# Optimization experiments

Measured on AMD Instinct MI355X. Metric: run time of the kernel, lower is better.

The kernel has to match this reference:

```python
import jax, jax.numpy as jnp
import numpy as np

B, S, I, H, P = 4096, 1024, 6, 128, 50  # batch, seq_len, input_size, hidden_size, predict_size


def setup_inputs() -> dict:
    key = jax.random.key(0)
    ks = jax.random.split(key, 12)
    k = 1.0 / np.sqrt(H)  # torch LSTM default init: U(-1/sqrt(H), 1/sqrt(H))
    u = lambda kk, shape: jax.random.uniform(kk, shape, jnp.float32, -k, k)
    # xavier_uniform for fc: bound = sqrt(6/(fan_in+fan_out))
    xb = np.sqrt(6.0 / (H + I))
    return {
        "x": jax.random.normal(ks[0], (B, S, I), jnp.float32),
        "w_ih0": u(ks[1], (4 * H, I)),
        "w_hh0": u(ks[2], (4 * H, H)),
        "b_ih0": u(ks[3], (4 * H,)),
        "b_hh0": u(ks[4], (4 * H,)),
        "w_ih1": u(ks[5], (4 * H, H)),
        "w_hh1": u(ks[6], (4 * H, H)),
        "b_ih1": u(ks[7], (4 * H,)),
        "b_hh1": u(ks[8], (4 * H,)),
        "fc_w": jax.random.uniform(ks[9], (I, H), jnp.float32, -xb, xb),
        "fc_b": jnp.full((I,), 0.01, jnp.float32),
    }


def _cell(xt, h, c, w_ih, w_hh, b):
    # gates: [i, f, g, o] stacked along last dim (torch order)
    g = xt @ w_ih.T + h @ w_hh.T + b
    i, f, gg, o = jnp.split(g, 4, axis=-1)
    c = jax.nn.sigmoid(f) * c + jax.nn.sigmoid(i) * jnp.tanh(gg)
    h = jax.nn.sigmoid(o) * jnp.tanh(c)
    return h, c


def reference(x, w_ih0, w_hh0, b_ih0, b_hh0, w_ih1, w_hh1, b_ih1, b_hh1, fc_w, fc_b):
    b0 = b_ih0 + b_hh0
    b1 = b_ih1 + b_hh1
    z = jnp.zeros((x.shape[0], H), x.dtype)

    def two_layer_step(carry, xt):
        h0, c0, h1, c1 = carry
        h0, c0 = _cell(xt, h0, c0, w_ih0, w_hh0, b0)
        h1, c1 = _cell(h0, h1, c1, w_ih1, w_hh1, b1)
        return (h0, c0, h1, c1), None

    # encode the input sequence; last top-layer output == final h1
    (h0, c0, h1, c1), _ = jax.lax.scan(two_layer_step, (z, z, z, z),
                                       jnp.swapaxes(x, 0, 1))  # (S,B,I)
    cur = jnp.tanh(h1 @ fc_w.T + fc_b)  # (B, I)

    def ar_step(carry, _):
        h0, c0, h1, c1, cur = carry
        h0, c0 = _cell(cur, h0, c0, w_ih0, w_hh0, b0)
        h1, c1 = _cell(h0, h1, c1, w_ih1, w_hh1, b1)
        pred = jnp.tanh(h1 @ fc_w.T + fc_b)
        return (h0, c0, h1, c1, pred), pred

    _, preds = jax.lax.scan(ar_step, (h0, c0, h1, c1, cur), None, length=P)
    return jnp.swapaxes(preds, 0, 1)  # (B, P, I)
```

## Files before the change

### kernel.cpp

```cpp
#include <hip/hip_runtime.h>

#define SEQ 1024
#define ISZ 6
#define HSZ 128
#define PRED 50
#define MROW 16
#define HP   136
#define XCH  8
#define WSB  131072

using f32x4  = __attribute__((ext_vector_type(4))) float;
using bf16x8 = __attribute__((ext_vector_type(8))) short;

__device__ __forceinline__ short f2bf(float f){
  union { float f; unsigned u; } v; v.f = f;
  unsigned r = v.u + 0x7FFFu + ((v.u >> 16) & 1u);
  return (short)(r >> 16);
}
__device__ __forceinline__ float bf2f(unsigned short us){
  union { unsigned u; float f; } v; v.u = ((unsigned)us) << 16; return v.f;
}
__device__ __forceinline__ float sigf(float x){
  float e = __builtin_amdgcn_exp2f(x * -1.4426950408889634f);
  return __builtin_amdgcn_rcpf(1.0f + e);
}
__device__ __forceinline__ float tanhf_(float x){
  float e = __builtin_amdgcn_exp2f(x * 2.8853900817779268f);
  return 1.0f - 2.0f * __builtin_amdgcn_rcpf(1.0f + e);
}

#define PIN(v) asm volatile("" : "+v"(v))

template<int PRECVT>
__global__
__attribute__((amdgpu_flat_work_group_size(512, 512)))
void lstm_ar(
    const float* __restrict__ x,
    const float* __restrict__ w_ih0, const float* __restrict__ w_hh0,
    const float* __restrict__ b_ih0, const float* __restrict__ b_hh0,
    const float* __restrict__ w_ih1, const float* __restrict__ w_hh1,
    const float* __restrict__ b_ih1, const float* __restrict__ b_hh1,
    const float* __restrict__ fc_w, const float* __restrict__ fc_b,
    float* __restrict__ out, unsigned short* __restrict__ wsb)
{
  __shared__ short s_whh1[65536];
  __shared__ short s_h0[2][MROW*HP];
  __shared__ short s_h1[MROW*HP];
  __shared__ short s_x[(XCH+1)*MROW*8];
  __shared__ short s_wih0[512*8];
  __shared__ float s_bias[2*512];
  __shared__ float s_fcb[8];
  __shared__ short s_zpad[8];

  const int tid  = threadIdx.x;
  const int wv   = tid >> 6;
  const int lane = tid & 63;
  const int l15  = lane & 15;
  const int lq   = lane >> 4;
  const int u    = wv*16 + l15;
  const int row0 = blockIdx.x * MROW;
  char* const whh1b = (char*)s_whh1;

  for (int i = tid; i < 2*MROW*HP; i += 512) (&s_h0[0][0])[i] = 0;
  for (int i = tid; i < MROW*HP;   i += 512) s_h1[i] = 0;
  for (int i = tid; i < (XCH+1)*MROW*8; i += 512) s_x[i] = 0;
  if (tid < 8){ s_zpad[tid] = 0; s_fcb[tid] = (tid < 6) ? fc_b[tid] : 0.f; }
  {
    #pragma unroll
    for (int k = 0; k < 6; k++) s_wih0[tid*8 + k] = f2bf(w_ih0[tid*6 + k]);
    s_wih0[tid*8 + 6] = 0; s_wih0[tid*8 + 7] = 0;
  }
  for (int i = tid; i < 1024; i += 512)
    s_bias[i] = (i < 512) ? (b_ih0[i] + b_hh0[i]) : (b_ih1[i-512] + b_hh1[i-512]);

  for (int i = tid; i < 32768; i += 512){
    const int c = i >> 6, kp = i & 63;
    const unsigned lo = (unsigned short)f2bf(w_hh1[c*128 + 2*kp]);
    const unsigned hi = (unsigned short)f2bf(w_hh1[c*128 + 2*kp + 1]);
    *(unsigned*)(whh1b + ((i*4) ^ ((c & 7) << 4))) = lo | (hi << 16);
  }

  if (PRECVT){
    #pragma unroll
    for (int g = 0; g < 4; g++){
      const int c = g*128 + u;
      #pragma unroll
      for (int kt = 0; kt < 4; kt++){
        const float* wp = w_hh0 + c*HSZ + kt*32 + lq*8;
        bf16x8 f;
        #pragma unroll
        for (int i = 0; i < 8; i++) f[i] = f2bf(wp[i]);
        *(bf16x8*)(wsb + (((wv*4 + g)*4 + kt)*64 + lane)*8) = f;
      }
    }
  }

  bf16x8 wih1f[4][4];
  #pragma unroll
  for (int g = 0; g < 4; g++){
    const int c = g*128 + u;
    #pragma unroll
    for (int kt = 0; kt < 4; kt++){
      const float* wp = w_ih1 + c*HSZ + kt*32 + lq*8;
      bf16x8 f;
      #pragma unroll
      for (int i = 0; i < 8; i++) f[i] = f2bf(wp[i]);
      wih1f[g][kt] = f;
    }
  }

  float c0[4] = {0.f,0.f,0.f,0.f}, c1[4] = {0.f,0.f,0.f,0.f};
  volatile const float* vb = s_bias;
  __syncthreads();

  for (int t = 0; t < SEQ + PRED; ++t){
    #pragma unroll
    for (int g = 0; g < 4; g++){
      #pragma unroll
      for (int kt = 0; kt < 4; kt++) PIN(wih1f[g][kt]);
    }

    if (t < SEQ && (t & (XCH-1)) == 0){
      for (int i = tid; i < XCH*MROW*ISZ; i += 512){
        const int r = i / (XCH*ISZ), rem = i % (XCH*ISZ);
        const int ts = rem / ISZ, k = rem % ISZ;
        s_x[(ts*MROW + r)*8 + k] =
          f2bf(x[(size_t)(row0 + r)*(SEQ*ISZ) + (size_t)(t + ts)*ISZ + k]);
      }
      __syncthreads();
    }
    const int tt = (t < SEQ) ? (t & (XCH-1)) : XCH;
    const int pb = t & 1, qb = pb ^ 1;

    const bf16x8 ax = *(const bf16x8*)((lq == 0) ? (s_x + (tt*MROW + l15)*8) : s_zpad);
    f32x4 acc[4];
    #pragma unroll
    for (int g = 0; g < 4; g++){
      const bf16x8 bw = *(const bf16x8*)((lq == 0) ? (s_wih0 + (g*128 + u)*8) : s_zpad);
      const float bg = vb[g*128 + u];
      f32x4 ci; ci[0] = bg; ci[1] = bg; ci[2] = bg; ci[3] = bg;
      acc[g] = __builtin_amdgcn_mfma_f32_16x16x32_bf16(ax, bw, ci, 0, 0, 0);
    }
    #pragma unroll
    for (int kt = 0; kt < 4; kt++){
      bf16x8 stg[4];
      if (PRECVT){
        #pragma unroll
        for (int g = 0; g < 4; g++)
          stg[g] = *(const bf16x8*)(wsb + (((wv*4 + g)*4 + kt)*64 + lane)*8);
      } else {
        #pragma unroll
        for (int g = 0; g < 4; g++){
          const float* wp = w_hh0 + (g*128 + u)*HSZ + kt*32 + lq*8;
          bf16x8 f;
          #pragma unroll
          for (int i = 0; i < 8; i++) f[i] = f2bf(wp[i]);
          stg[g] = f;
        }
      }
      const bf16x8 a = *(const bf16x8*)(s_h0[qb] + l15*HP + (kt*4 + lq)*8);
      #pragma unroll
      for (int g = 0; g < 4; g++)
        acc[g] = __builtin_amdgcn_mfma_f32_16x16x32_bf16(a, stg[g], acc[g], 0, 0, 0);
    }
    #pragma unroll
    for (int j = 0; j < 4; j++){
      const float iv = sigf(acc[0][j]);
      const float fv = sigf(acc[1][j]);
      const float gv = tanhf_(acc[2][j]);
      const float ov = sigf(acc[3][j]);
      c0[j] = fv*c0[j] + iv*gv;
      const float h = ov * tanhf_(c0[j]);
      s_h0[pb][(lq*4 + j)*HP + u] = f2bf(h);
    }
    __syncthreads();

    #pragma unroll
    for (int g = 0; g < 4; g++){
      const float bg = vb[512 + g*128 + u];
      acc[g][0] = bg; acc[g][1] = bg; acc[g][2] = bg; acc[g][3] = bg;
    }
    #pragma unroll
    for (int kt = 0; kt < 4; kt++){
      const bf16x8 a = *(const bf16x8*)(s_h0[pb] + l15*HP + (kt*4 + lq)*8);
      #pragma unroll
      for (int g = 0; g < 4; g++)
        acc[g] = __builtin_amdgcn_mfma_f32_16x16x32_bf16(a, wih1f[g][kt], acc[g], 0, 0, 0);
    }
    #pragma unroll
    for (int kt = 0; kt < 4; kt++){
      const bf16x8 a = *(const bf16x8*)(s_h1 + l15*HP + (kt*4 + lq)*8);
      #pragma unroll
      for (int g = 0; g < 4; g++){
        const int c = g*128 + u;
        const bf16x8 b = *(const bf16x8*)(whh1b +
            ((c*256 + (kt*4 + lq)*16) ^ ((u & 7) << 4)));
        acc[g] = __builtin_amdgcn_mfma_f32_16x16x32_bf16(a, b, acc[g], 0, 0, 0);
      }
    }
    __syncthreads();
    const bool dofc = (t >= SEQ - 1);
    #pragma unroll
    for (int j = 0; j < 4; j++){
      const float iv = sigf(acc[0][j]);
      const float fv = sigf(acc[1][j]);
      const float gv = tanhf_(acc[2][j]);
      const float ov = sigf(acc[3][j]);
      c1[j] = fv*c1[j] + iv*gv;
      const float h = ov * tanhf_(c1[j]);
      s_h1[(lq*4 + j)*HP + u] = f2bf(h);
    }

    if (dofc){
      __syncthreads();
      if (tid < 96){
        const int r = tid / 6, ii = tid % 6;
        float sacc = 0.f;
        #pragma unroll 4
        for (int kk = 0; kk < 128; kk++)
          sacc += bf2f((unsigned short)s_h1[r*HP + kk]) * fc_w[ii*128 + kk];
        const float pred = tanhf_(s_fcb[ii] + sacc);
        s_x[(XCH*MROW + r)*8 + ii] = f2bf(pred);
        if (t >= SEQ)
          out[(size_t)(row0 + r)*(PRED*ISZ) + (size_t)(t - SEQ)*ISZ + ii] = pred;
      }
      __syncthreads();
    }
  }
}

extern "C" void kernel_launch(void* const* d_in, const int* in_sizes, int n_in,
                              void* d_out, int out_size, void* d_ws, size_t ws_size,
                              hipStream_t stream) {
  const float* x     = (const float*)d_in[0];
  const float* w_ih0 = (const float*)d_in[1];
  const float* w_hh0 = (const float*)d_in[2];
  const float* b_ih0 = (const float*)d_in[3];
  const float* b_hh0 = (const float*)d_in[4];
  const float* w_ih1 = (const float*)d_in[5];
  const float* w_hh1 = (const float*)d_in[6];
  const float* b_ih1 = (const float*)d_in[7];
  const float* b_hh1 = (const float*)d_in[8];
  const float* fc_w  = (const float*)d_in[9];
  const float* fc_b  = (const float*)d_in[10];
  float* out = (float*)d_out;
  unsigned short* wsb = (unsigned short*)d_ws;

  const int Btot = in_sizes[0] / (SEQ * ISZ);
  const int nblk = Btot / MROW;

  if (ws_size >= (size_t)WSB)
    lstm_ar<1><<<dim3(nblk), dim3(512), 0, stream>>>(
        x, w_ih0, w_hh0, b_ih0, b_hh0, w_ih1, w_hh1, b_ih1, b_hh1,
        fc_w, fc_b, out, wsb);
  else
    lstm_ar<0><<<dim3(nblk), dim3(512), 0, stream>>>(
        x, w_ih0, w_hh0, b_ih0, b_hh0, w_ih1, w_hh1, b_ih1, b_hh1,
        fc_w, fc_b, out, wsb);
}
```

Before: 3.207 ms.

## Split LSTM layers into producer/consumer blocks pipelined through global-memory rings

```diff
diff --git a/kernel.cpp b/kernel.cpp
--- a/kernel.cpp
+++ b/kernel.cpp
@@ -7,7 +7,31 @@
 #define MROW 16
 #define HP   136
 #define XCH  8
-#define WSB  131072
+#define NS   2
+#define TSTEPS (SEQ + PRED)
+
+#define F_H0   ((size_t)0)
+#define F_CUR  ((size_t)32768)
+#define F_CONS ((size_t)65536)
+#define F_ABT  ((size_t)98304)
+#define FLAGBYTES ((size_t)98432)
+#define R_H0   FLAGBYTES
+#define R_CUR  (R_H0 + (size_t)256*NS*4096)
+#define R_W1   (R_CUR + (size_t)256*NS*256)
+#define WS_NEED (R_W1 + (size_t)65536)
+
+#define OW1    0
+#define OLAND  65536
+#define OH1    69888
+#define OFCW   74240
+#define OCT    77312
+#define OFCB   77568
+#define OZP1   77600
+#define OH0    0
+#define OX     8704
+#define OWIH0  10752
+#define OZP0   18944
+#define POOLB  77632
 
 using f32x4  = __attribute__((ext_vector_type(4))) float;
 using bf16x8 = __attribute__((ext_vector_type(8))) short;
@@ -28,13 +52,304 @@
   float e = __builtin_amdgcn_exp2f(x * 2.8853900817779268f);
   return 1.0f - 2.0f * __builtin_amdgcn_rcpf(1.0f + e);
 }
-
 #define PIN(v) asm volatile("" : "+v"(v))
+
+__device__ __forceinline__ int aldf(const int* p){
+  return __hip_atomic_load(p, __ATOMIC_ACQUIRE, __HIP_MEMORY_SCOPE_AGENT);
+}
+__device__ __forceinline__ void astf(int* p, int v){
+  __hip_atomic_store(p, v, __ATOMIC_RELEASE, __HIP_MEMORY_SCOPE_AGENT);
+}
+__device__ __forceinline__ unsigned long long ald64(const void* p){
+  return __hip_atomic_load((const unsigned long long*)p, __ATOMIC_RELAXED, __HIP_MEMORY_SCOPE_AGENT);
+}
+__device__ __forceinline__ void ast64(void* p, unsigned long long v){
+  __hip_atomic_store((unsigned long long*)p, v, __ATOMIC_RELAXED, __HIP_MEMORY_SCOPE_AGENT);
+}
+__device__ __forceinline__ void ast32(void* p, unsigned v){
+  __hip_atomic_store((unsigned*)p, v, __ATOMIC_RELAXED, __HIP_MEMORY_SCOPE_AGENT);
+}
+__device__ __forceinline__ void waitge(const int* f, int v, int* abt){
+  if (threadIdx.x == 0){
+    int n = 0;
+    while (aldf(f) < v){
+      if (aldf(abt)) break;
+      __builtin_amdgcn_s_sleep(8);
+      if (++n > (1 << 21)){ astf(abt, 1); break; }
+    }
+  }
+  __syncthreads();
+}
+
+__global__
+__attribute__((amdgpu_flat_work_group_size(512, 512)))
+void lstm_pipe(
+    const float* __restrict__ x,
+    const float* __restrict__ w_ih0, const float* __restrict__ w_hh0,
+    const float* __restrict__ b_ih0, const float* __restrict__ b_hh0,
+    const float* __restrict__ w_ih1, const float* __restrict__ w_hh1,
+    const float* __restrict__ b_ih1, const float* __restrict__ b_hh1,
+    const float* __restrict__ fc_w, const float* __restrict__ fc_b,
+    float* __restrict__ out, char* __restrict__ ws)
+{
+  __shared__ __align__(16) char pool[POOLB];
+
+  const int tid  = threadIdx.x;
+  const int wv   = tid >> 6;
+  const int lane = tid & 63;
+  const int l15  = lane & 15;
+  const int lq   = lane >> 4;
+  const int u    = wv*16 + l15;
+  const int type = blockIdx.x >> 8;
+  const int p    = blockIdx.x & 255;
+  const int row0 = p * MROW;
+
+  int* h0f     = (int*)(ws + F_H0   + (size_t)p*128);
+  int* curf    = (int*)(ws + F_CUR  + (size_t)p*128);
+  int* consf   = (int*)(ws + F_CONS + (size_t)p*128);
+  int* abt     = (int*)(ws + F_ABT);
+  char* h0ring = ws + R_H0  + (size_t)p*(NS*4096);
+  char* curring= ws + R_CUR + (size_t)p*(NS*256);
+  short* w1p   = (short*)(ws + R_W1);
+
+  if (type == 0){
+    short* s_h0   = (short*)(pool + OH0);
+    short* s_x    = (short*)(pool + OX);
+    short* s_wih0 = (short*)(pool + OWIH0);
+    short* s_zp   = (short*)(pool + OZP0);
+
+    for (int i = tid; i < 2*MROW*HP; i += 512) s_h0[i] = 0;
+    for (int i = tid; i < XCH*MROW*8; i += 512) s_x[i] = 0;
+    if (tid < 8) s_zp[tid] = 0;
+    {
+      #pragma unroll
+      for (int k = 0; k < 6; k++) s_wih0[tid*8 + k] = f2bf(w_ih0[tid*6 + k]);
+      s_wih0[tid*8 + 6] = 0; s_wih0[tid*8 + 7] = 0;
+    }
+    bf16x8 whh0f[4][4];
+    float bias0[4];
+    #pragma unroll
+    for (int g = 0; g < 4; g++){
+      const int c = g*128 + u;
+      bias0[g] = b_ih0[c] + b_hh0[c];
+      #pragma unroll
+      for (int kt = 0; kt < 4; kt++){
+        const float* wp = w_hh0 + c*HSZ + kt*32 + lq*8;
+        bf16x8 f;
+        #pragma unroll
+        for (int i = 0; i < 8; i++) f[i] = f2bf(wp[i]);
+        whh0f[g][kt] = f;
+      }
+    }
+    float c0[4] = {0.f,0.f,0.f,0.f};
+    __syncthreads();
+
+    for (int t = 0; t < TSTEPS; ++t){
+      #pragma unroll
+      for (int g = 0; g < 4; g++){
+        #pragma unroll
+        for (int kt = 0; kt < 4; kt++) PIN(whh0f[g][kt]);
+      }
+      if (t >= NS) waitge(consf, t - NS + 1, abt);
+
+      bf16x8 ax;
+      if (t < SEQ){
+        if ((t & (XCH-1)) == 0){
+          for (int i = tid; i < XCH*MROW*ISZ; i += 512){
+            const int r = i / (XCH*ISZ), rem = i % (XCH*ISZ);
+            const int ts = rem / ISZ, k = rem % ISZ;
+            s_x[(ts*MROW + r)*8 + k] =
+              f2bf(x[(size_t)(row0 + r)*(SEQ*ISZ) + (size_t)(t + ts)*ISZ + k]);
+          }
+          __syncthreads();
+        }
+        ax = *(const bf16x8*)((lq == 0) ? (s_x + ((t & (XCH-1))*MROW + l15)*8) : s_zp);
+      } else {
+        waitge(curf, t - SEQ + 1, abt);
+        if (lq == 0){
+          const char* cp = curring + ((t - SEQ) % NS)*256 + l15*16;
+          union { unsigned long long q[2]; bf16x8 v; } uu;
+          uu.q[0] = ald64(cp); uu.q[1] = ald64(cp + 8);
+          ax = uu.v;
+        } else ax = *(const bf16x8*)s_zp;
+      }
+
+      const int pb = t & 1, qb = pb ^ 1;
+      short* h0q = s_h0 + qb*(MROW*HP);
+      short* h0p = s_h0 + pb*(MROW*HP);
+      f32x4 acc[4];
+      #pragma unroll
+      for (int g = 0; g < 4; g++){
+        const bf16x8 bw = *(const bf16x8*)((lq == 0) ? (s_wih0 + (g*128 + u)*8) : s_zp);
+        f32x4 ci; ci[0]=bias0[g]; ci[1]=bias0[g]; ci[2]=bias0[g]; ci[3]=bias0[g];
+        acc[g] = __builtin_amdgcn_mfma_f32_16x16x32_bf16(ax, bw, ci, 0, 0, 0);
+      }
+      #pragma unroll
+      for (int kt = 0; kt < 4; kt++){
+        const bf16x8 a = *(const bf16x8*)(h0q + l15*HP + (kt*4 + lq)*8);
+        #pragma unroll
+        for (int g = 0; g < 4; g++)
+          acc[g] = __builtin_amdgcn_mfma_f32_16x16x32_bf16(a, whh0f[g][kt], acc[g], 0, 0, 0);
+      }
+      #pragma unroll
+      for (int j = 0; j < 4; j++){
+        const float iv = sigf(acc[0][j]);
+        const float fv = sigf(acc[1][j]);
+        const float gv = tanhf_(acc[2][j]);
+        const float ov = sigf(acc[3][j]);
+        c0[j] = fv*c0[j] + iv*gv;
+        const float h = ov * tanhf_(c0[j]);
+        h0p[(lq*4 + j)*HP + u] = f2bf(h);
+      }
+      __syncthreads();
+      {
+        unsigned long long v = *(const unsigned long long*)(h0p + (tid >> 5)*HP + (tid & 31)*4);
+        ast64(h0ring + (t % NS)*4096 + tid*8, v);
+      }
+      __syncthreads();
+      if (tid == 0) astf(h0f, t + 1);
+    }
+  } else {
+    char*  w1l   = pool + OW1;
+    short* s_land= (short*)(pool + OLAND);
+    short* s_h1  = (short*)(pool + OH1);
+    float* s_fcw = (float*)(pool + OFCW);
+    short* s_ct  = (short*)(pool + OCT);
+    float* s_fcb = (float*)(pool + OFCB);
+
+    for (int i = tid; i < 16384; i += 512){
+      const int c = i >> 5, kp = i & 31;
+      const unsigned lo = (unsigned short)f2bf(w_ih1[c*128 + 2*kp]);
+      const unsigned hi = (unsigned short)f2bf(w_ih1[c*128 + 2*kp + 1]);
+      *(unsigned*)(w1l + ((i*4) ^ ((c & 7) << 4))) = lo | (hi << 16);
+    }
+    #pragma unroll
+    for (int g = 0; g < 4; g++){
+      const int c = g*128 + u;
+      #pragma unroll
+      for (int ktl = 0; ktl < 2; ktl++){
+        const float* wp = w_ih1 + c*HSZ + (2 + ktl)*32 + lq*8;
+        bf16x8 f;
+        #pragma unroll
+        for (int i = 0; i < 8; i++) f[i] = f2bf(wp[i]);
+        *(bf16x8*)(w1p + (((wv*4 + g)*2 + ktl)*64 + lane)*8) = f;
+      }
+    }
+    bf16x8 whh1f[4][4];
+    float bias1[4];
+    #pragma unroll
+    for (int g = 0; g < 4; g++){
+      const int c = g*128 + u;
+      bias1[g] = b_ih1[c] + b_hh1[c];
+      #pragma unroll
+      for (int kt = 0; kt < 4; kt++){
+        const float* wp = w_hh1 + c*HSZ + kt*32 + lq*8;
+        bf16x8 f;
+        #pragma unroll
+        for (int i = 0; i < 8; i++) f[i] = f2bf(wp[i]);
+        whh1f[g][kt] = f;
+      }
+    }
+    for (int i = tid; i < MROW*HP; i += 512) s_h1[i] = 0;
+    for (int i = tid; i < ISZ*HSZ; i += 512) s_fcw[i] = fc_w[i];
+    if (tid < 8) s_fcb[tid] = (tid < 6) ? fc_b[tid] : 0.f;
+    if (tid < MROW*8) s_ct[tid] = 0;
+    float c1[4] = {0.f,0.f,0.f,0.f};
+    __syncthreads();
+
+    for (int t = 0; t < TSTEPS; ++t){
+      #pragma unroll
+      for (int g = 0; g < 4; g++){
+        #pragma unroll
+        for (int kt = 0; kt < 4; kt++) PIN(whh1f[g][kt]);
+      }
+      waitge(h0f, t + 1, abt);
+      {
+        unsigned long long v = ald64(h0ring + (t % NS)*4096 + tid*8);
+        *(unsigned long long*)(s_land + (tid >> 5)*HP + (tid & 31)*4) = v;
+      }
+      __syncthreads();
+      if (tid == 0) astf(consf, t + 1);
+
+      bf16x8 sA[4], sB[4];
+      #pragma unroll
+      for (int g = 0; g < 4; g++){
+        sA[g] = *(const bf16x8*)(w1p + (((wv*4 + g)*2 + 0)*64 + lane)*8);
+        sB[g] = *(const bf16x8*)(w1p + (((wv*4 + g)*2 + 1)*64 + lane)*8);
+      }
+      f32x4 acc[4];
+      #pragma unroll
+      for (int g = 0; g < 4; g++){
+        acc[g][0]=bias1[g]; acc[g][1]=bias1[g]; acc[g][2]=bias1[g]; acc[g][3]=bias1[g];
+      }
+      #pragma unroll
+      for (int kt = 0; kt < 2; kt++){
+        const bf16x8 a = *(const bf16x8*)(s_land + l15*HP + (kt*4 + lq)*8);
+        #pragma unroll
+        for (int g = 0; g < 4; g++){
+          const int c = g*128 + u;
+          const bf16x8 b = *(const bf16x8*)(w1l +
+              ((c*128 + (kt*4 + lq)*16) ^ ((u & 7) << 4)));
+          acc[g] = __builtin_amdgcn_mfma_f32_16x16x32_bf16(a, b, acc[g], 0, 0, 0);
+        }
+      }
+      #pragma unroll
+      for (int kt = 0; kt < 4; kt++){
+        const bf16x8 a = *(const bf16x8*)(s_h1 + l15*HP + (kt*4 + lq)*8);
+        #pragma unroll
+        for (int g = 0; g < 4; g++)
+          acc[g] = __builtin_amdgcn_mfma_f32_16x16x32_bf16(a, whh1f[g][kt], acc[g], 0, 0, 0);
+      }
+      {
+        const bf16x8 a2 = *(const bf16x8*)(s_land + l15*HP + (2*4 + lq)*8);
+        #pragma unroll
+        for (int g = 0; g < 4; g++)
+          acc[g] = __builtin_amdgcn_mfma_f32_16x16x32_bf16(a2, sA[g], acc[g], 0, 0, 0);
+        const bf16x8 a3 = *(const bf16x8*)(s_land + l15*HP + (3*4 + lq)*8);
+        #pragma unroll
+        for (int g = 0; g < 4; g++)
+          acc[g] = __builtin_amdgcn_mfma_f32_16x16x32_bf16(a3, sB[g], acc[g], 0, 0, 0);
+      }
+      __syncthreads();
+      const bool dofc = (t >= SEQ - 1);
+      #pragma unroll
+      for (int j = 0; j < 4; j++){
+        const float iv = sigf(acc[0][j]);
+        const float fv = sigf(acc[1][j]);
+        const float gv = tanhf_(acc[2][j]);
+        const float ov = sigf(acc[3][j]);
+        c1[j] = fv*c1[j] + iv*gv;
+        const float h = ov * tanhf_(c1[j]);
+        s_h1[(lq*4 + j)*HP + u] = f2bf(h);
+      }
+      if (dofc){
+        __syncthreads();
+        if (tid < 96){
+          const int r = tid / 6, ii = tid % 6;
+          float sacc = 0.f;
+          #pragma unroll 4
+          for (int kk = 0; kk < 128; kk++)
+            sacc += bf2f((unsigned short)s_h1[r*HP + kk]) * s_fcw[ii*128 + kk];
+          const float pred = tanhf_(s_fcb[ii] + sacc);
+          s_ct[r*8 + ii] = f2bf(pred);
+          if (t >= SEQ)
+            out[(size_t)(row0 + r)*(PRED*ISZ) + (size_t)(t - SEQ)*ISZ + ii] = pred;
+        }
+        if (tid < 16){ s_ct[tid*8 + 6] = 0; s_ct[tid*8 + 7] = 0; }
+        __syncthreads();
+        if (tid < 64)
+          ast32(curring + ((t - (SEQ-1)) % NS)*256 + tid*4, ((unsigned*)s_ct)[tid]);
+        __syncthreads();
+        if (tid == 0) astf(curf, t - SEQ + 2);
+      }
+    }
+  }
+}
 
 template<int PRECVT>
 __global__
 __attribute__((amdgpu_flat_work_group_size(512, 512)))
-void lstm_ar(
+void lstm_fb(
     const float* __restrict__ x,
     const float* __restrict__ w_ih0, const float* __restrict__ w_hh0,
     const float* __restrict__ b_ih0, const float* __restrict__ b_hh0,
@@ -72,14 +387,12 @@
   }
   for (int i = tid; i < 1024; i += 512)
     s_bias[i] = (i < 512) ? (b_ih0[i] + b_hh0[i]) : (b_ih1[i-512] + b_hh1[i-512]);
-
   for (int i = tid; i < 32768; i += 512){
     const int c = i >> 6, kp = i & 63;
     const unsigned lo = (unsigned short)f2bf(w_hh1[c*128 + 2*kp]);
     const unsigned hi = (unsigned short)f2bf(w_hh1[c*128 + 2*kp + 1]);
     *(unsigned*)(whh1b + ((i*4) ^ ((c & 7) << 4))) = lo | (hi << 16);
   }
-
   if (PRECVT){
     #pragma unroll
     for (int g = 0; g < 4; g++){
@@ -94,7 +407,6 @@
       }
     }
   }
-
   bf16x8 wih1f[4][4];
   #pragma unroll
   for (int g = 0; g < 4; g++){
@@ -108,18 +420,16 @@
       wih1f[g][kt] = f;
     }
   }
-
   float c0[4] = {0.f,0.f,0.f,0.f}, c1[4] = {0.f,0.f,0.f,0.f};
   volatile const float* vb = s_bias;
   __syncthreads();
 
-  for (int t = 0; t < SEQ + PRED; ++t){
+  for (int t = 0; t < TSTEPS; ++t){
     #pragma unroll
     for (int g = 0; g < 4; g++){
       #pragma unroll
       for (int kt = 0; kt < 4; kt++) PIN(wih1f[g][kt]);
     }
-
     if (t < SEQ && (t & (XCH-1)) == 0){
       for (int i = tid; i < XCH*MROW*ISZ; i += 512){
         const int r = i / (XCH*ISZ), rem = i % (XCH*ISZ);
@@ -210,7 +520,6 @@
       const float h = ov * tanhf_(c1[j]);
       s_h1[(lq*4 + j)*HP + u] = f2bf(h);
     }
-
     if (dofc){
       __syncthreads();
       if (tid < 96){
@@ -244,17 +553,23 @@
   const float* fc_w  = (const float*)d_in[9];
   const float* fc_b  = (const float*)d_in[10];
   float* out = (float*)d_out;
-  unsigned short* wsb = (unsigned short*)d_ws;
-
-  const int Btot = in_sizes[0] / (SEQ * ISZ);
-  const int nblk = Btot / MROW;
-
-  if (ws_size >= (size_t)WSB)
-    lstm_ar<1><<<dim3(nblk), dim3(512), 0, stream>>>(
+
+  int nb = 0;
+  hipError_t oe = hipOccupancyMaxActiveBlocksPerMultiprocessor(&nb, lstm_pipe, 512, 0);
+  const bool pipe_ok = (oe == hipSuccess) && (nb >= 2) && (ws_size >= WS_NEED);
+
+  if (pipe_ok){
+    hipMemsetAsync(d_ws, 0, FLAGBYTES, stream);
+    lstm_pipe<<<dim3(512), dim3(512), 0, stream>>>(
         x, w_ih0, w_hh0, b_ih0, b_hh0, w_ih1, w_hh1, b_ih1, b_hh1,
-        fc_w, fc_b, out, wsb);
-  else
-    lstm_ar<0><<<dim3(nblk), dim3(512), 0, stream>>>(
+        fc_w, fc_b, out, (char*)d_ws);
+  } else if (ws_size >= (size_t)131072){
+    lstm_fb<1><<<dim3(256), dim3(512), 0, stream>>>(
         x, w_ih0, w_hh0, b_ih0, b_hh0, w_ih1, w_hh1, b_ih1, b_hh1,
-        fc_w, fc_b, out, wsb);
-}
+        fc_w, fc_b, out, (unsigned short*)d_ws);
+  } else {
+    lstm_fb<0><<<dim3(256), dim3(512), 0, stream>>>(
+        x, w_ih0, w_hh0, b_ih0, b_hh0, w_ih1, w_hh1, b_ih1, b_hh1,
+        fc_w, fc_b, out, (unsigned short*)d_ws);
+  }
+}
```

After: 3.207 ms. About the same (-0.0%).

## Double-buffer layer-1 hidden state and overlap its recurrent matmul with layer 0

Applied to the files above, without the earlier changes.

```diff
diff --git a/kernel.cpp b/kernel.cpp
--- a/kernel.cpp
+++ b/kernel.cpp
@@ -7,7 +7,11 @@
 #define MROW 16
 #define HP   136
 #define XCH  8
-#define WSB  131072
+#define TSTEPS (SEQ + PRED)
+
+#define W0OFF 0
+#define W1OFF 65536
+#define WS_NEED ((size_t)196608)
 
 using f32x4  = __attribute__((ext_vector_type(4))) float;
 using bf16x8 = __attribute__((ext_vector_type(8))) short;
@@ -28,13 +32,12 @@
   float e = __builtin_amdgcn_exp2f(x * 2.8853900817779268f);
   return 1.0f - 2.0f * __builtin_amdgcn_rcpf(1.0f + e);
 }
-
 #define PIN(v) asm volatile("" : "+v"(v))
 
 template<int PRECVT>
 __global__
 __attribute__((amdgpu_flat_work_group_size(512, 512)))
-void lstm_ar(
+void lstm_m2(
     const float* __restrict__ x,
     const float* __restrict__ w_ih0, const float* __restrict__ w_hh0,
     const float* __restrict__ b_ih0, const float* __restrict__ b_hh0,
@@ -43,14 +46,14 @@
     const float* __restrict__ fc_w, const float* __restrict__ fc_b,
     float* __restrict__ out, unsigned short* __restrict__ wsb)
 {
-  __shared__ short s_whh1[65536];
-  __shared__ short s_h0[2][MROW*HP];
-  __shared__ short s_h1[MROW*HP];
-  __shared__ short s_x[(XCH+1)*MROW*8];
-  __shared__ short s_wih0[512*8];
-  __shared__ float s_bias[2*512];
+  __shared__ __align__(16) short s_whh1[65536];
+  __shared__ __align__(16) short s_h0[2][MROW*HP];
+  __shared__ __align__(16) short s_h1[2][MROW*HP];
+  __shared__ __align__(16) short s_x[(XCH+1)*MROW*8];
+  __shared__ __align__(16) short s_wih0[512*8];
+  __shared__ __align__(16) float s_bias[1024];
   __shared__ float s_fcb[8];
-  __shared__ short s_zpad[8];
+  __shared__ __align__(16) short s_zpad[8];
 
   const int tid  = threadIdx.x;
   const int wv   = tid >> 6;
@@ -60,9 +63,11 @@
   const int u    = wv*16 + l15;
   const int row0 = blockIdx.x * MROW;
   char* const whh1b = (char*)s_whh1;
+  unsigned short* const w0p = wsb + W0OFF;
+  unsigned short* const w1p = wsb + W1OFF;
 
   for (int i = tid; i < 2*MROW*HP; i += 512) (&s_h0[0][0])[i] = 0;
-  for (int i = tid; i < MROW*HP;   i += 512) s_h1[i] = 0;
+  for (int i = tid; i < 2*MROW*HP; i += 512) (&s_h1[0][0])[i] = 0;
   for (int i = tid; i < (XCH+1)*MROW*8; i += 512) s_x[i] = 0;
   if (tid < 8){ s_zpad[tid] = 0; s_fcb[tid] = (tid < 6) ? fc_b[tid] : 0.f; }
   {
@@ -72,14 +77,12 @@
   }
   for (int i = tid; i < 1024; i += 512)
     s_bias[i] = (i < 512) ? (b_ih0[i] + b_hh0[i]) : (b_ih1[i-512] + b_hh1[i-512]);
-
   for (int i = tid; i < 32768; i += 512){
     const int c = i >> 6, kp = i & 63;
     const unsigned lo = (unsigned short)f2bf(w_hh1[c*128 + 2*kp]);
     const unsigned hi = (unsigned short)f2bf(w_hh1[c*128 + 2*kp + 1]);
     *(unsigned*)(whh1b + ((i*4) ^ ((c & 7) << 4))) = lo | (hi << 16);
   }
-
   if (PRECVT){
     #pragma unroll
     for (int g = 0; g < 4; g++){
@@ -90,17 +93,24 @@
         bf16x8 f;
         #pragma unroll
         for (int i = 0; i < 8; i++) f[i] = f2bf(wp[i]);
-        *(bf16x8*)(wsb + (((wv*4 + g)*4 + kt)*64 + lane)*8) = f;
-      }
-    }
-  }
-
-  bf16x8 wih1f[4][4];
+        *(bf16x8*)(w0p + (((wv*4 + g)*4 + kt)*64 + lane)*8) = f;
+      }
+      #pragma unroll
+      for (int ktl = 0; ktl < 2; ktl++){
+        const float* wp = w_ih1 + c*HSZ + (2 + ktl)*32 + lq*8;
+        bf16x8 f;
+        #pragma unroll
+        for (int i = 0; i < 8; i++) f[i] = f2bf(wp[i]);
+        *(bf16x8*)(w1p + (((wv*4 + g)*2 + ktl)*64 + lane)*8) = f;
+      }
+    }
+  }
+  bf16x8 wih1f[4][2];
   #pragma unroll
   for (int g = 0; g < 4; g++){
     const int c = g*128 + u;
     #pragma unroll
-    for (int kt = 0; kt < 4; kt++){
+    for (int kt = 0; kt < 2; kt++){
       const float* wp = w_ih1 + c*HSZ + kt*32 + lq*8;
       bf16x8 f;
       #pragma unroll
@@ -113,12 +123,9 @@
   volatile const float* vb = s_bias;
   __syncthreads();
 
-  for (int t = 0; t < SEQ + PRED; ++t){
-    #pragma unroll
-    for (int g = 0; g < 4; g++){
-      #pragma unroll
-      for (int kt = 0; kt < 4; kt++) PIN(wih1f[g][kt]);
-    }
+  for (int t = 0; t < TSTEPS; ++t){
+    #pragma unroll
+    for (int g = 0; g < 4; g++){ PIN(wih1f[g][0]); PIN(wih1f[g][1]); }
 
     if (t < SEQ && (t & (XCH-1)) == 0){
       for (int i = tid; i < XCH*MROW*ISZ; i += 512){
@@ -131,15 +138,23 @@
     }
     const int tt = (t < SEQ) ? (t & (XCH-1)) : XCH;
     const int pb = t & 1, qb = pb ^ 1;
+    short* const h0q = &s_h0[qb][0];
+    short* const h0p = &s_h0[pb][0];
+    short* const h1q = &s_h1[qb][0];
+    short* const h1p = &s_h1[pb][0];
+
+    float b0t[4], b1t[4];
+    #pragma unroll
+    for (int g = 0; g < 4; g++){ b0t[g] = vb[g*128 + u]; b1t[g] = vb[512 + g*128 + u]; }
 
     const bf16x8 ax = *(const bf16x8*)((lq == 0) ? (s_x + (tt*MROW + l15)*8) : s_zpad);
-    f32x4 acc[4];
+    f32x4 acc0[4], acc1[4];
     #pragma unroll
     for (int g = 0; g < 4; g++){
       const bf16x8 bw = *(const bf16x8*)((lq == 0) ? (s_wih0 + (g*128 + u)*8) : s_zpad);
-      const float bg = vb[g*128 + u];
-      f32x4 ci; ci[0] = bg; ci[1] = bg; ci[2] = bg; ci[3] = bg;
-      acc[g] = __builtin_amdgcn_mfma_f32_16x16x32_bf16(ax, bw, ci, 0, 0, 0);
+      f32x4 ci; ci[0]=b0t[g]; ci[1]=b0t[g]; ci[2]=b0t[g]; ci[3]=b0t[g];
+      acc0[g] = __builtin_amdgcn_mfma_f32_16x16x32_bf16(ax, bw, ci, 0, 0, 0);
+      acc1[g][0]=b1t[g]; acc1[g][1]=b1t[g]; acc1[g][2]=b1t[g]; acc1[g][3]=b1t[g];
     }
     #pragma unroll
     for (int kt = 0; kt < 4; kt++){
@@ -147,7 +162,7 @@
       if (PRECVT){
         #pragma unroll
         for (int g = 0; g < 4; g++)
-          stg[g] = *(const bf16x8*)(wsb + (((wv*4 + g)*4 + kt)*64 + lane)*8);
+          stg[g] = *(const bf16x8*)(w0p + (((wv*4 + g)*4 + kt)*64 + lane)*8);
       } else {
         #pragma unroll
         for (int g = 0; g < 4; g++){
@@ -158,67 +173,84 @@
           stg[g] = f;
         }
       }
-      const bf16x8 a = *(const bf16x8*)(s_h0[qb] + l15*HP + (kt*4 + lq)*8);
-      #pragma unroll
-      for (int g = 0; g < 4; g++)
-        acc[g] = __builtin_amdgcn_mfma_f32_16x16x32_bf16(a, stg[g], acc[g], 0, 0, 0);
-    }
-    #pragma unroll
-    for (int j = 0; j < 4; j++){
-      const float iv = sigf(acc[0][j]);
-      const float fv = sigf(acc[1][j]);
-      const float gv = tanhf_(acc[2][j]);
-      const float ov = sigf(acc[3][j]);
-      c0[j] = fv*c0[j] + iv*gv;
-      const float h = ov * tanhf_(c0[j]);
-      s_h0[pb][(lq*4 + j)*HP + u] = f2bf(h);
-    }
-    __syncthreads();
-
-    #pragma unroll
-    for (int g = 0; g < 4; g++){
-      const float bg = vb[512 + g*128 + u];
-      acc[g][0] = bg; acc[g][1] = bg; acc[g][2] = bg; acc[g][3] = bg;
-    }
-    #pragma unroll
-    for (int kt = 0; kt < 4; kt++){
-      const bf16x8 a = *(const bf16x8*)(s_h0[pb] + l15*HP + (kt*4 + lq)*8);
-      #pragma unroll
-      for (int g = 0; g < 4; g++)
-        acc[g] = __builtin_amdgcn_mfma_f32_16x16x32_bf16(a, wih1f[g][kt], acc[g], 0, 0, 0);
-    }
-    #pragma unroll
-    for (int kt = 0; kt < 4; kt++){
-      const bf16x8 a = *(const bf16x8*)(s_h1 + l15*HP + (kt*4 + lq)*8);
+      const bf16x8 a1 = *(const bf16x8*)(h1q + l15*HP + (kt*4 + lq)*8);
       #pragma unroll
       for (int g = 0; g < 4; g++){
         const int c = g*128 + u;
         const bf16x8 b = *(const bf16x8*)(whh1b +
             ((c*256 + (kt*4 + lq)*16) ^ ((u & 7) << 4)));
-        acc[g] = __builtin_amdgcn_mfma_f32_16x16x32_bf16(a, b, acc[g], 0, 0, 0);
-      }
+        acc1[g] = __builtin_amdgcn_mfma_f32_16x16x32_bf16(a1, b, acc1[g], 0, 0, 0);
+      }
+      const bf16x8 a0 = *(const bf16x8*)(h0q + l15*HP + (kt*4 + lq)*8);
+      #pragma unroll
+      for (int g = 0; g < 4; g++)
+        acc0[g] = __builtin_amdgcn_mfma_f32_16x16x32_bf16(a0, stg[g], acc0[g], 0, 0, 0);
+    }
+    #pragma unroll
+    for (int j = 0; j < 4; j++){
+      const float iv = sigf(acc0[0][j]);
+      const float fv = sigf(acc0[1][j]);
+      const float gv = tanhf_(acc0[2][j]);
+      const float ov = sigf(acc0[3][j]);
+      c0[j] = fv*c0[j] + iv*gv;
+      const float h = ov * tanhf_(c0[j]);
+      h0p[(lq*4 + j)*HP + u] = f2bf(h);
     }
     __syncthreads();
+
+    bf16x8 sB[2][4];
+    if (PRECVT){
+      #pragma unroll
+      for (int ktl = 0; ktl < 2; ktl++)
+        #pragma unroll
+        for (int g = 0; g < 4; g++)
+          sB[ktl][g] = *(const bf16x8*)(w1p + (((wv*4 + g)*2 + ktl)*64 + lane)*8);
+    } else {
+      #pragma unroll
+      for (int ktl = 0; ktl < 2; ktl++)
+        #pragma unroll
+        for (int g = 0; g < 4; g++){
+          const float* wp = w_ih1 + (g*128 + u)*HSZ + (2 + ktl)*32 + lq*8;
+          bf16x8 f;
+          #pragma unroll
+          for (int i = 0; i < 8; i++) f[i] = f2bf(wp[i]);
+          sB[ktl][g] = f;
+        }
+    }
+    #pragma unroll
+    for (int kt = 0; kt < 2; kt++){
+      const bf16x8 a = *(const bf16x8*)(h0p + l15*HP + (kt*4 + lq)*8);
+      #pragma unroll
+      for (int g = 0; g < 4; g++)
+        acc1[g] = __builtin_amdgcn_mfma_f32_16x16x32_bf16(a, wih1f[g][kt], acc1[g], 0, 0, 0);
+    }
+    #pragma unroll
+    for (int ktl = 0; ktl < 2; ktl++){
+      const bf16x8 a = *(const bf16x8*)(h0p + l15*HP + ((2 + ktl)*4 + lq)*8);
+      #pragma unroll
+      for (int g = 0; g < 4; g++)
+        acc1[g] = __builtin_amdgcn_mfma_f32_16x16x32_bf16(a, sB[ktl][g], acc1[g], 0, 0, 0);
+    }
     const bool dofc = (t >= SEQ - 1);
     #pragma unroll
     for (int j = 0; j < 4; j++){
-      const float iv = sigf(acc[0][j]);
-      const float fv = sigf(acc[1][j]);
-      const float gv = tanhf_(acc[2][j]);
-      const float ov = sigf(acc[3][j]);
+      const float iv = sigf(acc1[0][j]);
+      const float fv = sigf(acc1[1][j]);
+      const float gv = tanhf_(acc1[2][j]);
+      const float ov = sigf(acc1[3][j]);
       c1[j] = fv*c1[j] + iv*gv;
       const float h = ov * tanhf_(c1[j]);
-      s_h1[(lq*4 + j)*HP + u] = f2bf(h);
-    }
+      h1p[(lq*4 + j)*HP + u] = f2bf(h);
+    }
+    __syncthreads();
 
     if (dofc){
-      __syncthreads();
       if (tid < 96){
         const int r = tid / 6, ii = tid % 6;
         float sacc = 0.f;
         #pragma unroll 4
         for (int kk = 0; kk < 128; kk++)
-          sacc += bf2f((unsigned short)s_h1[r*HP + kk]) * fc_w[ii*128 + kk];
+          sacc += bf2f((unsigned short)h1p[r*HP + kk]) * fc_w[ii*128 + kk];
         const float pred = tanhf_(s_fcb[ii] + sacc);
         s_x[(XCH*MROW + r)*8 + ii] = f2bf(pred);
         if (t >= SEQ)
@@ -244,17 +276,16 @@
   const float* fc_w  = (const float*)d_in[9];
   const float* fc_b  = (const float*)d_in[10];
   float* out = (float*)d_out;
-  unsigned short* wsb = (unsigned short*)d_ws;
 
   const int Btot = in_sizes[0] / (SEQ * ISZ);
   const int nblk = Btot / MROW;
 
-  if (ws_size >= (size_t)WSB)
-    lstm_ar<1><<<dim3(nblk), dim3(512), 0, stream>>>(
+  if (ws_size >= WS_NEED)
+    lstm_m2<1><<<dim3(nblk), dim3(512), 0, stream>>>(
         x, w_ih0, w_hh0, b_ih0, b_hh0, w_ih1, w_hh1, b_ih1, b_hh1,
-        fc_w, fc_b, out, wsb);
+        fc_w, fc_b, out, (unsigned short*)d_ws);
   else
-    lstm_ar<0><<<dim3(nblk), dim3(512), 0, stream>>>(
+    lstm_m2<0><<<dim3(nblk), dim3(512), 0, stream>>>(
         x, w_ih0, w_hh0, b_ih0, b_hh0, w_ih1, w_hh1, b_ih1, b_hh1,
-        fc_w, fc_b, out, wsb);
-}
+        fc_w, fc_b, out, (unsigned short*)d_ws);
+}
```

Result: faster. 3.142 ms (-2.0%).
